# Optimization experiments

Hardware: AMD Instinct MI355X
Metric: run time of the kernel (lower is better)

## Reference

```python
import jax, jax.numpy as jnp
import numpy as np
import math

B, S, D = 4, 1024, 1024
H = 16
NQ = 8
HEAD_DIM = D // H
ALPHA = 0.7


def setup_inputs() -> dict:
    key = jax.random.key(0)
    ks = jax.random.split(key, 11)
    s = 1.0 / math.sqrt(D)
    return {
        "query": jax.random.normal(ks[0], (B, S, D), jnp.float32),
        "key": jax.random.normal(ks[1], (B, S, D), jnp.float32),
        "value": jax.random.normal(ks[2], (B, S, D), jnp.float32),
        "Wq": jax.random.normal(ks[3], (D, D), jnp.float32) * s,
        "bq": jnp.zeros((D,), jnp.float32),
        "Wk": jax.random.normal(ks[4], (D, D), jnp.float32) * s,
        "bk": jnp.zeros((D,), jnp.float32),
        "Wv": jax.random.normal(ks[5], (D, D), jnp.float32) * s,
        "bv": jnp.zeros((D,), jnp.float32),
        "Wo": jax.random.normal(ks[6], (D, D), jnp.float32) * s,
        "bo": jnp.zeros((D,), jnp.float32),
    }


def _pairwise_entropy(query, key):
    # tanh-encode and take first NQ features: [B, S, NQ]
    q_enc = jnp.tanh(query)[:, :, :NQ]
    k_enc = jnp.tanh(key)[:, :, :NQ]
    # combined[b,i,j,:] = concat(q_enc[b,i], k_enc[b,j]) -> [B, S, S, 2*NQ]
    qi = jnp.broadcast_to(q_enc[:, :, None, :], (B, S, S, NQ))
    kj = jnp.broadcast_to(k_enc[:, None, :, :], (B, S, S, NQ))
    combined = jnp.concatenate([qi, kj], axis=-1)
    probs = jax.nn.softmax(combined, axis=-1)
    # von Neumann-style entropy with the module's 1e-8 epsilon
    entropy = -jnp.sum(probs * jnp.log(probs + 1e-8), axis=-1)  # [B, S, S]
    return entropy


def reference(query, key, value, Wq, bq, Wk, bk, Wv, bv, Wo, bo):
    # Linear projections (torch Linear: x @ W^T + b)
    Q = query @ Wq.T + bq
    K = key @ Wk.T + bk
    V = value @ Wv.T + bv
    # [B, H, S, head_dim]
    Qh = Q.reshape(B, S, H, HEAD_DIM).transpose(0, 2, 1, 3)
    Kh = K.reshape(B, S, H, HEAD_DIM).transpose(0, 2, 1, 3)
    Vh = V.reshape(B, S, H, HEAD_DIM).transpose(0, 2, 1, 3)
    classical = jnp.einsum('bhsd,bhtd->bhst', Qh, Kh) / math.sqrt(HEAD_DIM)
    quantum = _pairwise_entropy(query, key)  # [B, S, S]
    combined = ALPHA * classical.mean(axis=1) + (1.0 - ALPHA) * quantum
    attn = jax.nn.softmax(combined, axis=-1)  # [B, S, S]
    # shared attention across heads
    attended = jnp.einsum('bst,bhtd->bhsd', attn, Vh)
    attended = attended.transpose(0, 2, 1, 3).reshape(B, S, D)
    output = attended @ Wo.T + bo
    return output, attn
```

## Files before the change

### kernel.cpp

```cpp
#include <hip/hip_runtime.h>


typedef float f32x4 __attribute__((ext_vector_type(4)));
typedef short s16x8 __attribute__((ext_vector_type(8)));
typedef unsigned short u16;

#define Bc 4
#define Sc 1024
#define Dc 1024
#define NTOK (Bc * Sc)
#define CSCALE (0.7f / 128.0f)
#define ESCALE 0.3f

typedef void __attribute__((address_space(1))) as1_void;
typedef void __attribute__((address_space(3))) as3_void;

__device__ __forceinline__ u16 f2b(float f) {
  union { float f; unsigned u; } v; v.f = f;
  unsigned r = v.u + 0x7fffu + ((v.u >> 16) & 1u);
  return (u16)(r >> 16);
}

__device__ __forceinline__ void xcd_map(int& bx, int& by, int& bz) {
  const int gx = gridDim.x, gy = gridDim.y;
  const int nwg = gx * gy * gridDim.z;
  const int lid = blockIdx.x + gx * (blockIdx.y + gy * blockIdx.z);
  const int cpx = nwg >> 3;
  const int s = (lid & 7) * cpx + (lid >> 3);
  bx = s % gx; const int r = s / gx; by = r % gy; bz = r / gy;
}

__global__ __launch_bounds__(256) void cast_all(const float* __restrict__ q,
                                                const float* __restrict__ k,
                                                const float* __restrict__ v,
                                                const float* __restrict__ wq,
                                                const float* __restrict__ wk,
                                                const float* __restrict__ wv,
                                                const float* __restrict__ wo,
                                                u16* __restrict__ qx, u16* __restrict__ kx,
                                                u16* __restrict__ vx, u16* __restrict__ Wb) {
  const int i = blockIdx.x * 256 + threadIdx.x;
  const float* src; u16* dst; int off;
  if (i < 3145728) {
    const int t = i >> 20; off = i & 1048575;
    src = (t == 0) ? q : (t == 1) ? k : v;
    dst = (t == 0) ? qx : (t == 1) ? kx : vx;
  } else {
    const int j = i - 3145728; const int t = j >> 18; off = j & 262143;
    src = (t == 0) ? wq : (t == 1) ? wk : (t == 2) ? wv : wo;
    dst = Wb + (size_t)t * Dc * Dc;
  }
  float4 vv = reinterpret_cast<const float4*>(src)[off];
  reinterpret_cast<ushort4*>(dst)[off] =
      make_ushort4(f2b(vv.x), f2b(vv.y), f2b(vv.z), f2b(vv.w));
}

__global__ __launch_bounds__(256) void ent_agg(const float* __restrict__ q,
                                               const float* __restrict__ k,
                                               float* __restrict__ agg) {
  int r = blockIdx.x * 256 + threadIdx.x;
  if (r >= 2 * NTOK) return;
  const float* src = (r < NTOK) ? (q + (size_t)r * Dc) : (k + (size_t)(r - NTOK) * Dc);
  float A = 0.f, Sv = 0.f;
#pragma unroll
  for (int m = 0; m < 8; ++m) {
    float e = tanhf(src[m]);
    float a = __expf(e);
    A += a; Sv += a * e;
  }
  if (r < NTOK) { agg[r] = A; agg[NTOK + r] = Sv; }
  else          { agg[NTOK + r] = A; agg[3 * NTOK + (r - NTOK)] = Sv; }
}

template<int BM, int NL>
__device__ __forceinline__ void gemm3(const u16* __restrict__ A, const u16* __restrict__ Bt,
                                      int row0, int col0, f32x4 (*acc)[4]) {
  constexpr int MR = BM / 32;
  constexpr int ASZ = BM * 32;
  constexpr int BSZ = 128 * 32;
  constexpr int K = 1024, nk = 32;
  __shared__ __align__(16) u16 LA[3 * ASZ];
  __shared__ __align__(16) u16 LB[3 * BSZ];
  const int tid = threadIdx.x;
  const int lane = tid & 63, wave = tid >> 6;
  const int wr = wave >> 1, wc = wave & 1;
  const int fr = lane & 15, g = lane >> 4;

  const int rA0 = tid >> 2;
  const int slA0 = (tid & 3) ^ ((rA0 >> 1) & 3);
  const u16* gA0 = A + (size_t)(row0 + rA0) * K + slA0 * 8;
  const u16* gA1 = nullptr;
  if constexpr (BM == 128) {
    const int rA1 = rA0 + 64;
    const int slA1 = (tid & 3) ^ ((rA1 >> 1) & 3);
    gA1 = A + (size_t)(row0 + rA1) * K + slA1 * 8;
  }
  const int rB1 = rA0 + 64;
  const int slB1 = (tid & 3) ^ ((rB1 >> 1) & 3);
  const u16* gB0 = Bt + (size_t)(col0 + rA0) * K + slA0 * 8;
  const u16* gB1 = Bt + (size_t)(col0 + rB1) * K + slB1 * 8;

  int aoff[MR], boff[4];
#pragma unroll
  for (int i = 0; i < MR; ++i) {
    const int row = wr * (MR * 16) + i * 16 + fr;
    aoff[i] = row * 32 + ((g ^ ((row >> 1) & 3)) << 3);
  }
#pragma unroll
  for (int j = 0; j < 4; ++j) {
    const int row = wc * 64 + j * 16 + fr;
    boff[j] = row * 32 + ((g ^ ((row >> 1) & 3)) << 3);
  }

  auto stage = [&](int aofs, int bofs, int kt) {
    const int ko = kt * 32;
    __builtin_amdgcn_global_load_lds((const as1_void*)(gA0 + ko),
                                     (as3_void*)(&LA[aofs + tid * 8]), 16, 0, 0);
    if constexpr (BM == 128)
      __builtin_amdgcn_global_load_lds((const as1_void*)(gA1 + ko),
                                       (as3_void*)(&LA[aofs + (256 + tid) * 8]), 16, 0, 0);
    __builtin_amdgcn_global_load_lds((const as1_void*)(gB0 + ko),
                                     (as3_void*)(&LB[bofs + tid * 8]), 16, 0, 0);
    __builtin_amdgcn_global_load_lds((const as1_void*)(gB1 + ko),
                                     (as3_void*)(&LB[bofs + (256 + tid) * 8]), 16, 0, 0);
  };

  stage(0, 0, 0);
  stage(ASZ, BSZ, 1);
  if constexpr (NL == 4) asm volatile("s_waitcnt vmcnt(4)" ::: "memory");
  else                   asm volatile("s_waitcnt vmcnt(3)" ::: "memory");
  __builtin_amdgcn_s_barrier();
  __builtin_amdgcn_sched_barrier(0);

  int a0 = 0, a1 = ASZ, a2 = 2 * ASZ;
  int b0 = 0, b1 = BSZ, b2 = 2 * BSZ;
  for (int kt = 0; kt < nk; ++kt) {
    if (kt + 2 < nk) stage(a2, b2, kt + 2);
    s16x8 af[MR], bf[4];
#pragma unroll
    for (int i = 0; i < MR; ++i) af[i] = *reinterpret_cast<const s16x8*>(&LA[a0 + aoff[i]]);
#pragma unroll
    for (int j = 0; j < 4; ++j) bf[j] = *reinterpret_cast<const s16x8*>(&LB[b0 + boff[j]]);
#pragma unroll
    for (int i = 0; i < MR; ++i)
#pragma unroll
      for (int j = 0; j < 4; ++j)
        acc[i][j] = __builtin_amdgcn_mfma_f32_16x16x32_bf16(af[i], bf[j], acc[i][j], 0, 0, 0);
    if (kt + 1 < nk) {
      if (kt + 2 < nk) {
        if constexpr (NL == 4) asm volatile("s_waitcnt vmcnt(4)" ::: "memory");
        else                   asm volatile("s_waitcnt vmcnt(3)" ::: "memory");
      } else {
        asm volatile("s_waitcnt vmcnt(0)" ::: "memory");
      }
      __builtin_amdgcn_s_barrier();
      __builtin_amdgcn_sched_barrier(0);
    }
    int t = a0; a0 = a1; a1 = a2; a2 = t;
    t = b0; b0 = b1; b1 = b2; b2 = t;
  }
}

__global__ __launch_bounds__(256, 3) void gemm_proj(const u16* __restrict__ Xall,
                                                    const u16* __restrict__ Wall,
                                                    const float* __restrict__ biasq,
                                                    const float* __restrict__ biask,
                                                    const float* __restrict__ biasv,
                                                    u16* __restrict__ QKout,
                                                    u16* __restrict__ Vt) {
  int bx, by, z; xcd_map(bx, by, z);
  const int row0 = bx * 128, col0 = by * 128;
  const u16* A  = Xall + (size_t)z * NTOK * Dc;
  const u16* Bt = Wall + (size_t)z * Dc * Dc;
  f32x4 acc[4][4] = {};
  gemm3<128, 4>(A, Bt, row0, col0, acc);

  const int lane = threadIdx.x & 63, wave = threadIdx.x >> 6;
  const int wm = (wave >> 1) * 64, wn = (wave & 1) * 64;
  const int cr = (lane >> 4) * 4, cc = lane & 15;
  const float* bias = (z == 0) ? biasq : (z == 1) ? biask : biasv;
#pragma unroll
  for (int j = 0; j < 4; ++j) {
    const int gc = col0 + wn + j * 16 + cc;
    const float bb = bias[gc];
#pragma unroll
    for (int i = 0; i < 4; ++i) {
      const int gr = row0 + wm + i * 16 + cr;
      f32x4 v = acc[i][j];
      if (z < 2) {
        u16* dst = QKout + (size_t)z * NTOK * Dc + (size_t)gr * Dc + gc;
#pragma unroll
        for (int r = 0; r < 4; ++r) dst[(size_t)r * Dc] = f2b(v[r] + bb);
      } else {
        const int b = gr >> 10, t = gr & (Sc - 1);
        ushort4 o = make_ushort4(f2b(v[0] + bb), f2b(v[1] + bb), f2b(v[2] + bb), f2b(v[3] + bb));
        *reinterpret_cast<ushort4*>(Vt + (size_t)b * Dc * Sc + (size_t)gc * Sc + t) = o;
      }
    }
  }
}

__global__ __launch_bounds__(256, 4) void gemm_scores(const u16* __restrict__ Qb,
                                                      const u16* __restrict__ Kb,
                                                      const float* __restrict__ agg,
                                                      float* __restrict__ comb) {
  int bx, by, z; xcd_map(bx, by, z);
  const int row0 = bx * 64, col0 = by * 128;
  const u16* A  = Qb + (size_t)z * Sc * Dc;
  const u16* Bt = Kb + (size_t)z * Sc * Dc;
  f32x4 acc[2][4] = {};
  gemm3<64, 3>(A, Bt, row0, col0, acc);

  const int lane = threadIdx.x & 63, wave = threadIdx.x >> 6;
  const int wm = (wave >> 1) * 32, wn = (wave & 1) * 64;
  const int cr = (lane >> 4) * 4, cc = lane & 15;
  const float* qA = agg + (size_t)z * Sc;
  const float* qS = agg + NTOK + (size_t)z * Sc;
  const float* kA = agg + 2 * NTOK + (size_t)z * Sc;
  const float* kS = agg + 3 * NTOK + (size_t)z * Sc;
  float* C = comb + (size_t)z * Sc * Sc;
#pragma unroll
  for (int j = 0; j < 4; ++j) {
    const int gc = col0 + wn + j * 16 + cc;
    const float kAv = kA[gc], kSv = kS[gc];
#pragma unroll
    for (int i = 0; i < 2; ++i) {
      const int gr = row0 + wm + i * 16 + cr;
      f32x4 v = acc[i][j];
#pragma unroll
      for (int r = 0; r < 4; ++r) {
        const int s = gr + r;
        const float Z = qA[s] + kAv;
        const float ent = __logf(Z) - (qS[s] + kSv) / Z;
        C[(size_t)s * Sc + gc] = CSCALE * v[r] + ESCALE * ent;
      }
    }
  }
}

__global__ __launch_bounds__(256) void softmax_row(const float* __restrict__ comb,
                                                   float* __restrict__ attn_f,
                                                   u16* __restrict__ attn_b) {
  const int row = blockIdx.x;
  const int t = threadIdx.x;
  const float* src = comb + (size_t)row * Sc;
  float4 v = reinterpret_cast<const float4*>(src)[t];
  float m = fmaxf(fmaxf(v.x, v.y), fmaxf(v.z, v.w));
#pragma unroll
  for (int off = 1; off < 64; off <<= 1) m = fmaxf(m, __shfl_xor(m, off));
  __shared__ float red[8];
  if ((t & 63) == 0) red[t >> 6] = m;
  __syncthreads();
  m = fmaxf(fmaxf(red[0], red[1]), fmaxf(red[2], red[3]));
  float e0 = __expf(v.x - m), e1 = __expf(v.y - m), e2 = __expf(v.z - m), e3 = __expf(v.w - m);
  float s = e0 + e1 + e2 + e3;
#pragma unroll
  for (int off = 1; off < 64; off <<= 1) s += __shfl_xor(s, off);
  if ((t & 63) == 0) red[4 + (t >> 6)] = s;
  __syncthreads();
  s = red[4] + red[5] + red[6] + red[7];
  const float inv = 1.f / s;
  float4 o = make_float4(e0 * inv, e1 * inv, e2 * inv, e3 * inv);
  reinterpret_cast<float4*>(attn_f + (size_t)row * Sc)[t] = o;
  ushort4 ob = make_ushort4(f2b(o.x), f2b(o.y), f2b(o.z), f2b(o.w));
  reinterpret_cast<ushort4*>(attn_b + (size_t)row * Sc)[t] = ob;
}

__global__ __launch_bounds__(256, 4) void gemm_av(const u16* __restrict__ attnb,
                                                  const u16* __restrict__ Vt,
                                                  u16* __restrict__ att) {
  int bx, by, z; xcd_map(bx, by, z);
  const int row0 = bx * 64, col0 = by * 128;
  const u16* A  = attnb + (size_t)z * Sc * Sc;
  const u16* Bt = Vt + (size_t)z * Dc * Sc;
  f32x4 acc[2][4] = {};
  gemm3<64, 3>(A, Bt, row0, col0, acc);

  const int lane = threadIdx.x & 63, wave = threadIdx.x >> 6;
  const int wm = (wave >> 1) * 32, wn = (wave & 1) * 64;
  const int cr = (lane >> 4) * 4, cc = lane & 15;
  u16* C = att + (size_t)z * Sc * Dc;
#pragma unroll
  for (int j = 0; j < 4; ++j) {
    const int gc = col0 + wn + j * 16 + cc;
#pragma unroll
    for (int i = 0; i < 2; ++i) {
      const int gr = row0 + wm + i * 16 + cr;
      f32x4 v = acc[i][j];
#pragma unroll
      for (int r = 0; r < 4; ++r) C[(size_t)(gr + r) * Dc + gc] = f2b(v[r]);
    }
  }
}

__global__ __launch_bounds__(256, 4) void gemm_out(const u16* __restrict__ att,
                                                   const u16* __restrict__ Wob,
                                                   const float* __restrict__ bo,
                                                   float* __restrict__ out) {
  int bx, by, bz; xcd_map(bx, by, bz);
  const int row0 = bx * 64, col0 = by * 128;
  f32x4 acc[2][4] = {};
  gemm3<64, 3>(att, Wob, row0, col0, acc);

  const int lane = threadIdx.x & 63, wave = threadIdx.x >> 6;
  const int wm = (wave >> 1) * 32, wn = (wave & 1) * 64;
  const int cr = (lane >> 4) * 4, cc = lane & 15;
#pragma unroll
  for (int j = 0; j < 4; ++j) {
    const int gc = col0 + wn + j * 16 + cc;
    const float bb = bo[gc];
#pragma unroll
    for (int i = 0; i < 2; ++i) {
      const int gr = row0 + wm + i * 16 + cr;
      f32x4 v = acc[i][j];
#pragma unroll
      for (int r = 0; r < 4; ++r) out[(size_t)(gr + r) * Dc + gc] = v[r] + bb;
    }
  }
}

extern "C" void kernel_launch(void* const* d_in, const int* in_sizes, int n_in,
                              void* d_out, int out_size, void* d_ws, size_t ws_size,
                              hipStream_t stream) {
  const float* query = (const float*)d_in[0];
  const float* key   = (const float*)d_in[1];
  const float* value = (const float*)d_in[2];
  const float* Wq = (const float*)d_in[3];
  const float* bq = (const float*)d_in[4];
  const float* Wk = (const float*)d_in[5];
  const float* bk = (const float*)d_in[6];
  const float* Wv = (const float*)d_in[7];
  const float* bv = (const float*)d_in[8];
  const float* Wo = (const float*)d_in[9];
  const float* bo = (const float*)d_in[10];

  float* out    = (float*)d_out;
  float* attn_f = out + (size_t)NTOK * Dc;

  char* w = (char*)d_ws;
  const size_t MB = 1ull << 20;
  u16* qx = (u16*)(w);
  u16* kx = (u16*)(w + 8 * MB);
  u16* vx = (u16*)(w + 16 * MB);
  float* comb = (float*)(w);
  u16* attnb  = (u16*)(w + 16 * MB);
  u16* Qb = (u16*)(w + 24 * MB);
  u16* attended = (u16*)(w + 24 * MB);
  u16* Vt = (u16*)(w + 40 * MB);
  u16* Wb = (u16*)(w + 48 * MB);
  float* agg = (float*)(w + 56 * MB);

  cast_all<<<16384, 256, 0, stream>>>(query, key, value, Wq, Wk, Wv, Wo, qx, kx, vx, Wb);

  ent_agg<<<(2 * NTOK) / 256, 256, 0, stream>>>(query, key, agg);

  gemm_proj<<<dim3(32, 8, 3), 256, 0, stream>>>(qx, Wb, bq, bk, bv, Qb, Vt);

  gemm_scores<<<dim3(16, 8, 4), 256, 0, stream>>>(Qb, Qb + (size_t)NTOK * Dc, agg, comb);

  softmax_row<<<NTOK, 256, 0, stream>>>(comb, attn_f, attnb);

  gemm_av<<<dim3(16, 8, 4), 256, 0, stream>>>(attnb, Vt, attended);

  gemm_out<<<dim3(64, 8, 1), 256, 0, stream>>>(attended, Wb + 3ull * Dc * Dc, bo, out);

  (void)in_sizes; (void)n_in; (void)out_size; (void)ws_size;
}
```

Before: 233.6 us.

## Use 8-wave GEMM blocks, LDS-staged V transpose, and column-major XCD mapping

The shared GEMM core now runs with 512 threads (8 waves in a 2x4 layout) per block. Each wave owns half as many output columns, and one 16-byte global-to-LDS load per thread covers each operand tile, so per-wave register pressure drops and more waves are available to hide latency. The V projection epilogue stages its tile in shared memory and writes the transposed Vt with contiguous vector stores, replacing scattered 8-byte stores. The XCD block mapping now walks the column index fastest, which changes L2 reuse. The risks are more barrier overhead, with more waves synchronising per k-step, and the different tile-to-XCD assignment.

```diff
diff --git a/kernel.cpp b/kernel.cpp
--- a/kernel.cpp
+++ b/kernel.cpp
@@ -27,7 +27,7 @@
   const int lid = blockIdx.x + gx * (blockIdx.y + gy * blockIdx.z);
   const int cpx = nwg >> 3;
   const int s = (lid & 7) * cpx + (lid >> 3);
-  bx = s % gx; const int r = s / gx; by = r % gy; bz = r / gy;
+  by = s % gy; const int r = s / gy; bx = r % gx; bz = r / gx;
 }
 
 __global__ __launch_bounds__(256) void cast_all(const float* __restrict__ q,
@@ -72,147 +72,159 @@
   else          { agg[NTOK + r] = A; agg[3 * NTOK + (r - NTOK)] = Sv; }
 }
 
-template<int BM, int NL>
-__device__ __forceinline__ void gemm3(const u16* __restrict__ A, const u16* __restrict__ Bt,
-                                      int row0, int col0, f32x4 (*acc)[4]) {
+template<int BM>
+__device__ __forceinline__ void gemm8(const u16* __restrict__ A, const u16* __restrict__ Bt,
+                                      int row0, int col0, f32x4 (*acc)[2],
+                                      u16* __restrict__ smem) {
   constexpr int MR = BM / 32;
   constexpr int ASZ = BM * 32;
   constexpr int BSZ = 128 * 32;
   constexpr int K = 1024, nk = 32;
-  __shared__ __align__(16) u16 LA[3 * ASZ];
-  __shared__ __align__(16) u16 LB[3 * BSZ];
+  u16* LA = smem;
+  u16* LB = smem + 3 * ASZ;
   const int tid = threadIdx.x;
   const int lane = tid & 63, wave = tid >> 6;
-  const int wr = wave >> 1, wc = wave & 1;
+  const int wr = wave >> 2, wc = wave & 3;
   const int fr = lane & 15, g = lane >> 4;
 
-  const int rA0 = tid >> 2;
-  const int slA0 = (tid & 3) ^ ((rA0 >> 1) & 3);
-  const u16* gA0 = A + (size_t)(row0 + rA0) * K + slA0 * 8;
-  const u16* gA1 = nullptr;
-  if constexpr (BM == 128) {
-    const int rA1 = rA0 + 64;
-    const int slA1 = (tid & 3) ^ ((rA1 >> 1) & 3);
-    gA1 = A + (size_t)(row0 + rA1) * K + slA1 * 8;
-  }
-  const int rB1 = rA0 + 64;
-  const int slB1 = (tid & 3) ^ ((rB1 >> 1) & 3);
-  const u16* gB0 = Bt + (size_t)(col0 + rA0) * K + slA0 * 8;
-  const u16* gB1 = Bt + (size_t)(col0 + rB1) * K + slB1 * 8;
-
-  int aoff[MR], boff[4];
+  const int rS = tid >> 2;
+  const int slS = (tid & 3) ^ ((rS >> 1) & 3);
+  const int rA = (BM == 128) ? rS : (rS & 63);
+  const u16* gB = Bt + (size_t)(col0 + rS) * K + slS * 8;
+  const u16* gA = A + (size_t)(row0 + rA) * K + slS * 8;
+
+  int aoff[MR], boff[2];
 #pragma unroll
   for (int i = 0; i < MR; ++i) {
     const int row = wr * (MR * 16) + i * 16 + fr;
     aoff[i] = row * 32 + ((g ^ ((row >> 1) & 3)) << 3);
   }
 #pragma unroll
-  for (int j = 0; j < 4; ++j) {
-    const int row = wc * 64 + j * 16 + fr;
+  for (int j = 0; j < 2; ++j) {
+    const int row = wc * 32 + j * 16 + fr;
     boff[j] = row * 32 + ((g ^ ((row >> 1) & 3)) << 3);
   }
 
-  auto stage = [&](int aofs, int bofs, int kt) {
+  auto stage = [&](int idx, int kt) {
     const int ko = kt * 32;
-    __builtin_amdgcn_global_load_lds((const as1_void*)(gA0 + ko),
-                                     (as3_void*)(&LA[aofs + tid * 8]), 16, 0, 0);
-    if constexpr (BM == 128)
-      __builtin_amdgcn_global_load_lds((const as1_void*)(gA1 + ko),
-                                       (as3_void*)(&LA[aofs + (256 + tid) * 8]), 16, 0, 0);
-    __builtin_amdgcn_global_load_lds((const as1_void*)(gB0 + ko),
-                                     (as3_void*)(&LB[bofs + tid * 8]), 16, 0, 0);
-    __builtin_amdgcn_global_load_lds((const as1_void*)(gB1 + ko),
-                                     (as3_void*)(&LB[bofs + (256 + tid) * 8]), 16, 0, 0);
+    if (BM == 128 || tid < 256)
+      __builtin_amdgcn_global_load_lds((const as1_void*)(gA + ko),
+                                       (as3_void*)(&LA[idx * ASZ + tid * 8]), 16, 0, 0);
+    __builtin_amdgcn_global_load_lds((const as1_void*)(gB + ko),
+                                     (as3_void*)(&LB[idx * BSZ + tid * 8]), 16, 0, 0);
   };
-
-  stage(0, 0, 0);
-  stage(ASZ, BSZ, 1);
-  if constexpr (NL == 4) asm volatile("s_waitcnt vmcnt(4)" ::: "memory");
-  else                   asm volatile("s_waitcnt vmcnt(3)" ::: "memory");
+  auto wait_nl = [&]() {
+    if constexpr (BM == 128) {
+      asm volatile("s_waitcnt vmcnt(2)" ::: "memory");
+    } else {
+      if (tid < 256) asm volatile("s_waitcnt vmcnt(2)" ::: "memory");
+      else           asm volatile("s_waitcnt vmcnt(1)" ::: "memory");
+    }
+  };
+
+  stage(0, 0);
+  stage(1, 1);
+  wait_nl();
   __builtin_amdgcn_s_barrier();
   __builtin_amdgcn_sched_barrier(0);
 
-  int a0 = 0, a1 = ASZ, a2 = 2 * ASZ;
-  int b0 = 0, b1 = BSZ, b2 = 2 * BSZ;
+  int c0 = 0, c1 = 1, c2 = 2;
   for (int kt = 0; kt < nk; ++kt) {
-    if (kt + 2 < nk) stage(a2, b2, kt + 2);
-    s16x8 af[MR], bf[4];
-#pragma unroll
-    for (int i = 0; i < MR; ++i) af[i] = *reinterpret_cast<const s16x8*>(&LA[a0 + aoff[i]]);
-#pragma unroll
-    for (int j = 0; j < 4; ++j) bf[j] = *reinterpret_cast<const s16x8*>(&LB[b0 + boff[j]]);
+    if (kt + 2 < nk) stage(c2, kt + 2);
+    const int ab = c0 * ASZ, bb = c0 * BSZ;
+    s16x8 af[MR], bfr[2];
+#pragma unroll
+    for (int i = 0; i < MR; ++i) af[i] = *reinterpret_cast<const s16x8*>(&LA[ab + aoff[i]]);
+#pragma unroll
+    for (int j = 0; j < 2; ++j) bfr[j] = *reinterpret_cast<const s16x8*>(&LB[bb + boff[j]]);
 #pragma unroll
     for (int i = 0; i < MR; ++i)
 #pragma unroll
-      for (int j = 0; j < 4; ++j)
-        acc[i][j] = __builtin_amdgcn_mfma_f32_16x16x32_bf16(af[i], bf[j], acc[i][j], 0, 0, 0);
+      for (int j = 0; j < 2; ++j)
+        acc[i][j] = __builtin_amdgcn_mfma_f32_16x16x32_bf16(af[i], bfr[j], acc[i][j], 0, 0, 0);
     if (kt + 1 < nk) {
-      if (kt + 2 < nk) {
-        if constexpr (NL == 4) asm volatile("s_waitcnt vmcnt(4)" ::: "memory");
-        else                   asm volatile("s_waitcnt vmcnt(3)" ::: "memory");
-      } else {
-        asm volatile("s_waitcnt vmcnt(0)" ::: "memory");
-      }
+      if (kt + 2 < nk) wait_nl();
+      else asm volatile("s_waitcnt vmcnt(0)" ::: "memory");
       __builtin_amdgcn_s_barrier();
       __builtin_amdgcn_sched_barrier(0);
     }
-    int t = a0; a0 = a1; a1 = a2; a2 = t;
-    t = b0; b0 = b1; b1 = b2; b2 = t;
-  }
-}
-
-__global__ __launch_bounds__(256, 3) void gemm_proj(const u16* __restrict__ Xall,
+    int t = c0; c0 = c1; c1 = c2; c2 = t;
+  }
+}
+
+__global__ __launch_bounds__(512, 6) void gemm_proj(const u16* __restrict__ Xall,
                                                     const u16* __restrict__ Wall,
                                                     const float* __restrict__ biasq,
                                                     const float* __restrict__ biask,
                                                     const float* __restrict__ biasv,
                                                     u16* __restrict__ QKout,
                                                     u16* __restrict__ Vt) {
+  __shared__ __align__(16) u16 smem[3 * (128 * 32) * 2];
   int bx, by, z; xcd_map(bx, by, z);
   const int row0 = bx * 128, col0 = by * 128;
   const u16* A  = Xall + (size_t)z * NTOK * Dc;
   const u16* Bt = Wall + (size_t)z * Dc * Dc;
-  f32x4 acc[4][4] = {};
-  gemm3<128, 4>(A, Bt, row0, col0, acc);
-
-  const int lane = threadIdx.x & 63, wave = threadIdx.x >> 6;
-  const int wm = (wave >> 1) * 64, wn = (wave & 1) * 64;
+  f32x4 acc[4][2] = {};
+  gemm8<128>(A, Bt, row0, col0, acc, smem);
+
+  const int tid = threadIdx.x;
+  const int lane = tid & 63, wave = tid >> 6;
+  const int wr = wave >> 2, wc = wave & 3;
   const int cr = (lane >> 4) * 4, cc = lane & 15;
   const float* bias = (z == 0) ? biasq : (z == 1) ? biask : biasv;
-#pragma unroll
-  for (int j = 0; j < 4; ++j) {
-    const int gc = col0 + wn + j * 16 + cc;
-    const float bb = bias[gc];
-#pragma unroll
-    for (int i = 0; i < 4; ++i) {
-      const int gr = row0 + wm + i * 16 + cr;
-      f32x4 v = acc[i][j];
-      if (z < 2) {
+  if (z < 2) {
+#pragma unroll
+    for (int j = 0; j < 2; ++j) {
+      const int gc = col0 + wc * 32 + j * 16 + cc;
+      const float bb = bias[gc];
+#pragma unroll
+      for (int i = 0; i < 4; ++i) {
+        const int gr = row0 + wr * 64 + i * 16 + cr;
+        f32x4 v = acc[i][j];
         u16* dst = QKout + (size_t)z * NTOK * Dc + (size_t)gr * Dc + gc;
 #pragma unroll
         for (int r = 0; r < 4; ++r) dst[(size_t)r * Dc] = f2b(v[r] + bb);
-      } else {
-        const int b = gr >> 10, t = gr & (Sc - 1);
+      }
+    }
+  } else {
+    __syncthreads();
+    u16* T = smem;
+#pragma unroll
+    for (int j = 0; j < 2; ++j) {
+      const int lc = wc * 32 + j * 16 + cc;
+      const float bb = bias[col0 + lc];
+#pragma unroll
+      for (int i = 0; i < 4; ++i) {
+        const int lrb = wr * 64 + i * 16 + cr;
+        f32x4 v = acc[i][j];
         ushort4 o = make_ushort4(f2b(v[0] + bb), f2b(v[1] + bb), f2b(v[2] + bb), f2b(v[3] + bb));
-        *reinterpret_cast<ushort4*>(Vt + (size_t)b * Dc * Sc + (size_t)gc * Sc + t) = o;
+        *reinterpret_cast<ushort4*>(&T[lc * 132 + lrb]) = o;
       }
     }
-  }
-}
-
-__global__ __launch_bounds__(256, 4) void gemm_scores(const u16* __restrict__ Qb,
+    __syncthreads();
+    const int d = tid >> 2, q = tid & 3;
+    const int b = row0 >> 10, t0 = row0 & (Sc - 1);
+    u16* dst = Vt + (size_t)b * Dc * Sc + (size_t)(col0 + d) * Sc + t0 + q * 32;
+#pragma unroll
+    for (int m = 0; m < 8; ++m)
+      reinterpret_cast<ushort4*>(dst)[m] = *reinterpret_cast<const ushort4*>(&T[d * 132 + q * 32 + m * 4]);
+  }
+}
+
+__global__ __launch_bounds__(512, 4) void gemm_scores(const u16* __restrict__ Qb,
                                                       const u16* __restrict__ Kb,
                                                       const float* __restrict__ agg,
                                                       float* __restrict__ comb) {
+  __shared__ __align__(16) u16 smem[3 * (64 * 32) + 3 * (128 * 32)];
   int bx, by, z; xcd_map(bx, by, z);
   const int row0 = bx * 64, col0 = by * 128;
   const u16* A  = Qb + (size_t)z * Sc * Dc;
   const u16* Bt = Kb + (size_t)z * Sc * Dc;
-  f32x4 acc[2][4] = {};
-  gemm3<64, 3>(A, Bt, row0, col0, acc);
+  f32x4 acc[2][2] = {};
+  gemm8<64>(A, Bt, row0, col0, acc, smem);
 
   const int lane = threadIdx.x & 63, wave = threadIdx.x >> 6;
-  const int wm = (wave >> 1) * 32, wn = (wave & 1) * 64;
+  const int wr = wave >> 2, wc = wave & 3;
   const int cr = (lane >> 4) * 4, cc = lane & 15;
   const float* qA = agg + (size_t)z * Sc;
   const float* qS = agg + NTOK + (size_t)z * Sc;
@@ -220,12 +232,12 @@
   const float* kS = agg + 3 * NTOK + (size_t)z * Sc;
   float* C = comb + (size_t)z * Sc * Sc;
 #pragma unroll
-  for (int j = 0; j < 4; ++j) {
-    const int gc = col0 + wn + j * 16 + cc;
+  for (int j = 0; j < 2; ++j) {
+    const int gc = col0 + wc * 32 + j * 16 + cc;
     const float kAv = kA[gc], kSv = kS[gc];
 #pragma unroll
     for (int i = 0; i < 2; ++i) {
-      const int gr = row0 + wm + i * 16 + cr;
+      const int gr = row0 + wr * 32 + i * 16 + cr;
       f32x4 v = acc[i][j];
 #pragma unroll
       for (int r = 0; r < 4; ++r) {
@@ -266,26 +278,27 @@
   reinterpret_cast<ushort4*>(attn_b + (size_t)row * Sc)[t] = ob;
 }
 
-__global__ __launch_bounds__(256, 4) void gemm_av(const u16* __restrict__ attnb,
+__global__ __launch_bounds__(512, 4) void gemm_av(const u16* __restrict__ attnb,
                                                   const u16* __restrict__ Vt,
                                                   u16* __restrict__ att) {
+  __shared__ __align__(16) u16 smem[3 * (64 * 32) + 3 * (128 * 32)];
   int bx, by, z; xcd_map(bx, by, z);
   const int row0 = bx * 64, col0 = by * 128;
   const u16* A  = attnb + (size_t)z * Sc * Sc;
   const u16* Bt = Vt + (size_t)z * Dc * Sc;
-  f32x4 acc[2][4] = {};
-  gemm3<64, 3>(A, Bt, row0, col0, acc);
+  f32x4 acc[2][2] = {};
+  gemm8<64>(A, Bt, row0, col0, acc, smem);
 
   const int lane = threadIdx.x & 63, wave = threadIdx.x >> 6;
-  const int wm = (wave >> 1) * 32, wn = (wave & 1) * 64;
+  const int wr = wave >> 2, wc = wave & 3;
   const int cr = (lane >> 4) * 4, cc = lane & 15;
   u16* C = att + (size_t)z * Sc * Dc;
 #pragma unroll
-  for (int j = 0; j < 4; ++j) {
-    const int gc = col0 + wn + j * 16 + cc;
+  for (int j = 0; j < 2; ++j) {
+    const int gc = col0 + wc * 32 + j * 16 + cc;
 #pragma unroll
     for (int i = 0; i < 2; ++i) {
-      const int gr = row0 + wm + i * 16 + cr;
+      const int gr = row0 + wr * 32 + i * 16 + cr;
       f32x4 v = acc[i][j];
 #pragma unroll
       for (int r = 0; r < 4; ++r) C[(size_t)(gr + r) * Dc + gc] = f2b(v[r]);
@@ -293,25 +306,26 @@
   }
 }
 
-__global__ __launch_bounds__(256, 4) void gemm_out(const u16* __restrict__ att,
+__global__ __launch_bounds__(512, 4) void gemm_out(const u16* __restrict__ att,
                                                    const u16* __restrict__ Wob,
                                                    const float* __restrict__ bo,
                                                    float* __restrict__ out) {
+  __shared__ __align__(16) u16 smem[3 * (64 * 32) + 3 * (128 * 32)];
   int bx, by, bz; xcd_map(bx, by, bz);
   const int row0 = bx * 64, col0 = by * 128;
-  f32x4 acc[2][4] = {};
-  gemm3<64, 3>(att, Wob, row0, col0, acc);
+  f32x4 acc[2][2] = {};
+  gemm8<64>(att, Wob, row0, col0, acc, smem);
 
   const int lane = threadIdx.x & 63, wave = threadIdx.x >> 6;
-  const int wm = (wave >> 1) * 32, wn = (wave & 1) * 64;
+  const int wr = wave >> 2, wc = wave & 3;
   const int cr = (lane >> 4) * 4, cc = lane & 15;
 #pragma unroll
-  for (int j = 0; j < 4; ++j) {
-    const int gc = col0 + wn + j * 16 + cc;
+  for (int j = 0; j < 2; ++j) {
+    const int gc = col0 + wc * 32 + j * 16 + cc;
     const float bb = bo[gc];
 #pragma unroll
     for (int i = 0; i < 2; ++i) {
-      const int gr = row0 + wm + i * 16 + cr;
+      const int gr = row0 + wr * 32 + i * 16 + cr;
       f32x4 v = acc[i][j];
 #pragma unroll
       for (int r = 0; r < 4; ++r) out[(size_t)(gr + r) * Dc + gc] = v[r] + bb;
@@ -354,15 +368,15 @@
 
   ent_agg<<<(2 * NTOK) / 256, 256, 0, stream>>>(query, key, agg);
 
-  gemm_proj<<<dim3(32, 8, 3), 256, 0, stream>>>(qx, Wb, bq, bk, bv, Qb, Vt);
-
-  gemm_scores<<<dim3(16, 8, 4), 256, 0, stream>>>(Qb, Qb + (size_t)NTOK * Dc, agg, comb);
+  gemm_proj<<<dim3(32, 8, 3), 512, 0, stream>>>(qx, Wb, bq, bk, bv, Qb, Vt);
+
+  gemm_scores<<<dim3(16, 8, 4), 512, 0, stream>>>(Qb, Qb + (size_t)NTOK * Dc, agg, comb);
 
   softmax_row<<<NTOK, 256, 0, stream>>>(comb, attn_f, attnb);
 
-  gemm_av<<<dim3(16, 8, 4), 256, 0, stream>>>(attnb, Vt, attended);
-
-  gemm_out<<<dim3(64, 8, 1), 256, 0, stream>>>(attended, Wb + 3ull * Dc * Dc, bo, out);
+  gemm_av<<<dim3(16, 8, 4), 512, 0, stream>>>(attnb, Vt, attended);
+
+  gemm_out<<<dim3(64, 8, 1), 512, 0, stream>>>(attended, Wb + 3ull * Dc * Dc, bo, out);
 
   (void)in_sizes; (void)n_in; (void)out_size; (void)ws_size;
 }
```

Result: faster. 226.1 us (-3.2%).
